# Performance work log

Measured on AMD Instinct MI355X. Metric: run time of the kernel, lower is better.

## Reference

```python
import jax, jax.numpy as jnp
import numpy as np

DIM = 512
NUM_HEADS = 8
HEAD_DIM = DIM // NUM_HEADS
KERNEL = (3, 5, 5)  # (kd, kh, kw), must be odd and <= spatial dims
B, D, H, W = 1, 6, 48, 96


def setup_inputs() -> dict:
    key = jax.random.key(0)
    ks = jax.random.split(key, 5)
    x = jax.random.normal(ks[0], (B, D, H, W, DIM), jnp.float32)
    w_qkv = jax.random.normal(ks[1], (DIM, 3 * DIM), jnp.float32) * 0.02
    b_qkv = jax.random.normal(ks[2], (3 * DIM,), jnp.float32) * 0.02
    w_proj = jax.random.normal(ks[3], (DIM, DIM), jnp.float32) * 0.02
    b_proj = jax.random.normal(ks[4], (DIM,), jnp.float32) * 0.02
    return {"x": x, "w_qkv": w_qkv, "b_qkv": b_qkv, "w_proj": w_proj, "b_proj": b_proj}


def _nbhd_idx(L, k):
    # NATTEN neighborhood: window of exactly k keys, centered, shifted inward at edges.
    p = jnp.arange(L)
    start = jnp.clip(p - k // 2, 0, L - k)
    return start[:, None] + jnp.arange(k)[None, :]  # [L, k]


def _na3d(q, k, v, kernel):
    # q, k, v: [B, D, H, W, heads, hd]; q pre-scaled.
    kd, kh, kw = kernel
    _, Dd, Hh, Ww, _, _ = q.shape
    idx_d = _nbhd_idx(Dd, kd)
    idx_h = _nbhd_idx(Hh, kh)
    idx_w = _nbhd_idx(Ww, kw)
    offs = jnp.stack(
        jnp.meshgrid(jnp.arange(kd), jnp.arange(kh), jnp.arange(kw), indexing="ij"),
        axis=-1,
    ).reshape(-1, 3)  # [K3, 3]

    def shift(t, o):
        # gather the o-th neighbor of every query position along each spatial axis
        t = jnp.take(t, jnp.take(idx_d, o[0], axis=1), axis=1)
        t = jnp.take(t, jnp.take(idx_h, o[1], axis=1), axis=2)
        t = jnp.take(t, jnp.take(idx_w, o[2], axis=1), axis=3)
        return t

    def score_step(_, o):
        k_s = shift(k, o)
        s = jnp.einsum("bdhwnc,bdhwnc->bdhwn", q, k_s)
        return None, s

    _, scores = jax.lax.scan(score_step, None, offs)  # [K3, B, D, H, W, heads]
    attn = jax.nn.softmax(scores, axis=0)

    def out_step(acc, xs):
        o, a = xs
        v_s = shift(v, o)
        return acc + a[..., None] * v_s, None

    out, _ = jax.lax.scan(out_step, jnp.zeros_like(q), (offs, attn))
    return out


def reference(x, w_qkv, b_qkv, w_proj, b_proj):
    Bb, Dd, Hh, Ww, C = x.shape
    qkv = (x @ w_qkv + b_qkv).reshape(Bb, Dd, Hh, Ww, 3, NUM_HEADS, HEAD_DIM)
    q = qkv[..., 0, :, :]
    k = qkv[..., 1, :, :]
    v = qkv[..., 2, :, :]
    scale = HEAD_DIM ** (-0.5)
    # Faithful to source: module scales q by self.scale, then tuned_na3d applies
    # head_dim**-0.5 again inside the fused kernel -> net q * head_dim**-1.
    q = q * (scale * scale)
    out = _na3d(q, k, v, KERNEL).reshape(Bb, Dd, Hh, Ww, C)
    return out @ w_proj + b_proj
```

## Files before the change

### kernel.cpp

```cpp
#include <hip/hip_runtime.h>

#define DIMC   512
#define NHEADS 8
#define HDIM   64
#define DD     6
#define HHH    48
#define WWW    96
#define NPOS   (DD * HHH * WWW)

typedef unsigned short u16;
typedef __attribute__((ext_vector_type(8))) short bf16x8;
typedef __attribute__((ext_vector_type(4))) float f32x4;

static __device__ __forceinline__ float b2f(u16 u) {
    return __builtin_bit_cast(float, (unsigned)u << 16);
}
static __device__ __forceinline__ u16 f2b(float f) {
    unsigned x = __builtin_bit_cast(unsigned, f);
    return (u16)((x + 0x7fffu + ((x >> 16) & 1u)) >> 16);
}

static __device__ __forceinline__ void gload_lds16(const void* g, void* l) {
    __builtin_amdgcn_global_load_lds((const __attribute__((address_space(1))) void*)g,
                                     (__attribute__((address_space(3))) void*)l, 16, 0, 0);
}

__global__ __launch_bounds__(256) void cvt_all(
    const float* __restrict__ x, const float* __restrict__ w_qkv,
    const float* __restrict__ w_proj, u16* __restrict__ xb,
    u16* __restrict__ wqkvT, u16* __restrict__ wprojT)
{
    const int bid = blockIdx.x;
    const int tid = threadIdx.x;
    if (bid < 13824) {
        const int i = bid * 256 + tid;
        float4 v = reinterpret_cast<const float4*>(x)[i];
        ushort4 o = { f2b(v.x), f2b(v.y), f2b(v.z), f2b(v.w) };
        reinterpret_cast<ushort4*>(xb)[i] = o;
    } else if (bid < 13824 + 3072) {
        const int id = (bid - 13824) * 256 + tid;
        const int nn = id >> 9, kk = id & 511;
        wqkvT[id] = f2b(w_qkv[(size_t)kk * 1536 + nn]);
    } else {
        const int id = (bid - 16896) * 256 + tid;
        const int nn = id >> 9, kk = id & 511;
        wprojT[id] = f2b(w_proj[(size_t)kk * 512 + nn]);
    }
}

__global__ __launch_bounds__(512) void gemm_bf16_mfma(
    const u16* __restrict__ A, int lda,
    const u16* __restrict__ B, int ldb,
    const float* __restrict__ bias, int Kp,
    void* __restrict__ Cout, int ldc, int cmode, int nx)
{
    __shared__ u16 As[256 * 64];
    __shared__ u16 Bs[128 * 64];

    const int tid = threadIdx.x;
    const int l   = tid & 63;
    const int w   = tid >> 6;
    const int wr  = w >> 1;
    const int wc  = w & 1;

    const int cpx = gridDim.x >> 3;
    const int idp = (blockIdx.x & 7) * cpx + (blockIdx.x >> 3);
    const int by  = idp / nx;
    const int bx  = idp - by * nx;
    const int m0  = by * 256;
    const int n0  = bx * 128;

    const int lrow = l >> 3;
    const int swz  = ((l & 7) ^ lrow) * 8;
    const int arow = w * 32 + lrow;
    const int brow = w * 16 + lrow;

    const u16* ga = A + (size_t)(m0 + arow) * lda + swz;
    const u16* gb = B + (size_t)(n0 + brow) * ldb + swz;
    const size_t a8 = (size_t)8 * lda;
    const size_t b8 = (size_t)8 * ldb;
    u16* const la0 = As + w * 2048;
    u16* const lb0 = Bs + w * 1024;

    f32x4 acc[4][4];
#pragma unroll
    for (int i = 0; i < 4; i++)
#pragma unroll
        for (int j = 0; j < 4; j++) acc[i][j] = (f32x4)0.0f;

    const int c   = l & 15;
    const int g   = l >> 4;
    const int lk0 = ((0 * 4 + g) ^ (c & 7)) * 8;
    const int lk1 = ((1 * 4 + g) ^ (c & 7)) * 8;

#pragma unroll 1
    for (int k0 = 0; k0 < Kp; k0 += 64) {
#pragma unroll
        for (int q = 0; q < 4; ++q)
            gload_lds16(ga + q * a8, la0 + q * 512);
#pragma unroll
        for (int q = 0; q < 2; ++q)
            gload_lds16(gb + q * b8, lb0 + q * 512);
        ga += 64; gb += 64;
        __syncthreads();

        {
            bf16x8 af[4], bfr[4];
#pragma unroll
            for (int f = 0; f < 4; f++) {
                af[f]  = *reinterpret_cast<const bf16x8*>(&As[(wr * 64 + f * 16 + c) * 64 + lk0]);
                bfr[f] = *reinterpret_cast<const bf16x8*>(&Bs[(wc * 64 + f * 16 + c) * 64 + lk0]);
            }
#pragma unroll
            for (int i = 0; i < 4; i++)
#pragma unroll
                for (int j = 0; j < 4; j++)
                    acc[i][j] = __builtin_amdgcn_mfma_f32_16x16x32_bf16(af[i], bfr[j], acc[i][j], 0, 0, 0);
        }
        {
            bf16x8 af[4], bfr[4];
#pragma unroll
            for (int f = 0; f < 4; f++) {
                af[f]  = *reinterpret_cast<const bf16x8*>(&As[(wr * 64 + f * 16 + c) * 64 + lk1]);
                bfr[f] = *reinterpret_cast<const bf16x8*>(&Bs[(wc * 64 + f * 16 + c) * 64 + lk1]);
            }
#pragma unroll
            for (int i = 0; i < 4; i++)
#pragma unroll
                for (int j = 0; j < 4; j++)
                    acc[i][j] = __builtin_amdgcn_mfma_f32_16x16x32_bf16(af[i], bfr[j], acc[i][j], 0, 0, 0);
        }
        __syncthreads();
    }

#pragma unroll
    for (int i = 0; i < 4; i++) {
        const int mb = m0 + wr * 64 + i * 16 + g * 4;
#pragma unroll
        for (int j = 0; j < 4; j++) {
            const int n = n0 + wc * 64 + j * 16 + c;
            const float bv = bias[n];
            const float scn = (cmode && n < 512) ? 0.022542110f : 1.0f;
#pragma unroll
            for (int r = 0; r < 4; r++) {
                const float v = (acc[i][j][r] + bv) * scn;
                if (cmode) reinterpret_cast<u16*>(Cout)[(size_t)(mb + r) * ldc + n] = f2b(v);
                else       reinterpret_cast<float*>(Cout)[(size_t)(mb + r) * ldc + n] = v;
            }
        }
    }
}

__global__ __launch_bounds__(512, 4) void na3d_mfma(
    const u16* __restrict__ qkv, u16* __restrict__ attnc)
{
    __shared__ int   rowoff[256];
    __shared__ int   dlt[16];
    __shared__ u16   Vt[NHEADS][64][36];
    __shared__ float ssum_lds[NHEADS][2][16];

    const int bid = blockIdx.x;
    const int x   = bid & 7;
    const int u   = bid >> 3;
    const int twl = u / 36;
    const int r2  = u - twl * 36;
    const int d0  = r2 / 12;
    const int thp = r2 - d0 * 12;
    const int h0  = thp * 4;
    const int w0  = (3 * x + twl) * 4;
    const int sdu = min(max(2 * d0 - 1, 0), DD - 4);
    const int shb = min(max(h0 - 2, 0), HHH - 5);
    const int swb = min(max(w0 - 2, 0), WWW - 5);
    const int ddlt0 = min(max(2 * d0 - 1, 0), DD - 3) - sdu;
    const int ddlt1 = min(max(2 * d0, 0), DD - 3) - sdu;

    const int tid = threadIdx.x;
    if (tid < 256) {
        const int dd = tid >> 6, hh = (tid >> 3) & 7, wu = tid & 7;
        const int row = (sdu + dd) * (HHH * WWW)
                      + min(shb + hh, HHH - 1) * WWW + min(swb + wu, WWW - 1);
        rowoff[tid] = row * 1536;
    }
    if (tid < 16) {
        const int ph = h0 + (tid >> 2), pw = w0 + (tid & 3);
        const int dh = min(max(ph - 2, 0), HHH - 5) - shb;
        const int dw = min(max(pw - 2, 0), WWW - 5) - swb;
        dlt[tid] = (dh << 4) | dw;
    }
    __syncthreads();

    const int head = tid >> 6;
    const int l    = tid & 63;
    const int g    = l >> 4;
    const int c    = l & 15;

    const int qbase = (h0 + (c >> 2)) * WWW + (w0 + (c & 3));
    const u16* qrow0 = qkv + (size_t)((2 * d0)     * (HHH * WWW) + qbase) * 1536 + head * HDIM;
    const u16* qrow1 = qkv + (size_t)((2 * d0 + 1) * (HHH * WWW) + qbase) * 1536 + head * HDIM;
    const bf16x8 qlo0 = *reinterpret_cast<const bf16x8*>(qrow0 + 8 * g);
    const bf16x8 qhi0 = *reinterpret_cast<const bf16x8*>(qrow0 + 32 + 8 * g);
    const bf16x8 qlo1 = *reinterpret_cast<const bf16x8*>(qrow1 + 8 * g);
    const bf16x8 qhi1 = *reinterpret_cast<const bf16x8*>(qrow1 + 32 + 8 * g);
    const int dparts = dlt[c];
    const int dh = dparts >> 4, dw = dparts & 15;

    f32x4 oacc0[4], oacc1[4];
#pragma unroll
    for (int j = 0; j < 4; j++) { oacc0[j] = (f32x4)0.0f; oacc1[j] = (f32x4)0.0f; }
    float ssum0 = 0.0f, ssum1 = 0.0f;

#pragma unroll 1
    for (int s = 0; s < 8; ++s) {
        {
            const int npair = l >> 2;
            const int chq   = l & 3;
#pragma unroll
            for (int rr = 0; rr < 2; ++rr) {
                const int ch8 = 8 * chq + 32 * rr;
                const int2 rp = *reinterpret_cast<const int2*>(&rowoff[s * 32 + 2 * npair]);
                const ushort4* pa = reinterpret_cast<const ushort4*>(qkv + rp.x + 1024 + head * HDIM + ch8);
                const ushort4* pb = reinterpret_cast<const ushort4*>(qkv + rp.y + 1024 + head * HDIM + ch8);
                ushort4 va0 = pa[0], va1 = pa[1];
                ushort4 vb0 = pb[0], vb1 = pb[1];
                const u16* va = reinterpret_cast<const u16*>(&va0);
                const u16* vb = reinterpret_cast<const u16*>(&vb0);
#pragma unroll
                for (int e = 0; e < 4; ++e) {
                    unsigned dwo = (unsigned)va[e] | ((unsigned)vb[e] << 16);
                    *reinterpret_cast<unsigned*>(&Vt[head][ch8 + e][2 * npair]) = dwo;
                }
                const u16* va2 = reinterpret_cast<const u16*>(&va1);
                const u16* vb2 = reinterpret_cast<const u16*>(&vb1);
#pragma unroll
                for (int e = 0; e < 4; ++e) {
                    unsigned dwo = (unsigned)va2[e] | ((unsigned)vb2[e] << 16);
                    *reinterpret_cast<unsigned*>(&Vt[head][ch8 + 4 + e][2 * npair]) = dwo;
                }
            }
        }

        f32x4 sf00 = (f32x4)0.0f, sf01 = (f32x4)0.0f;
        f32x4 sf10 = (f32x4)0.0f, sf11 = (f32x4)0.0f;
        {
            const int ro = rowoff[s * 32 + c];
            const u16* kr = qkv + ro + 512 + head * HDIM;
            const bf16x8 klo = *reinterpret_cast<const bf16x8*>(kr + 8 * g);
            const bf16x8 khi = *reinterpret_cast<const bf16x8*>(kr + 32 + 8 * g);
            sf00 = __builtin_amdgcn_mfma_f32_16x16x32_bf16(klo, qlo0, sf00, 0, 0, 0);
            sf00 = __builtin_amdgcn_mfma_f32_16x16x32_bf16(khi, qhi0, sf00, 0, 0, 0);
            sf01 = __builtin_amdgcn_mfma_f32_16x16x32_bf16(klo, qlo1, sf01, 0, 0, 0);
            sf01 = __builtin_amdgcn_mfma_f32_16x16x32_bf16(khi, qhi1, sf01, 0, 0, 0);
        }
        {
            const int ro = rowoff[s * 32 + 16 + c];
            const u16* kr = qkv + ro + 512 + head * HDIM;
            const bf16x8 klo = *reinterpret_cast<const bf16x8*>(kr + 8 * g);
            const bf16x8 khi = *reinterpret_cast<const bf16x8*>(kr + 32 + 8 * g);
            sf10 = __builtin_amdgcn_mfma_f32_16x16x32_bf16(klo, qlo0, sf10, 0, 0, 0);
            sf10 = __builtin_amdgcn_mfma_f32_16x16x32_bf16(khi, qhi0, sf10, 0, 0, 0);
            sf11 = __builtin_amdgcn_mfma_f32_16x16x32_bf16(klo, qlo1, sf11, 0, 0, 0);
            sf11 = __builtin_amdgcn_mfma_f32_16x16x32_bf16(khi, qhi1, sf11, 0, 0, 0);
        }

        const int sbA  = s * 32 + 4 * g;
        const int sbB  = sbA + 16;
        const int ddA  = sbA >> 6, hhA = (sbA >> 3) & 7, wuA = sbA & 7;
        const int ddB  = sbB >> 6, hhB = (sbB >> 3) & 7, wuB = sbB & 7;
        const bool hvA = ((unsigned)(hhA - dh) < 5u);
        const bool hvB = ((unsigned)(hhB - dh) < 5u);

        unsigned pA0, pB0, pC0, pD0, pA1, pB1, pC1, pD1;
#define EXPPACK(sf, dvA_, pX, pY, SSUM, hv_, wu_) do {                          \
    const bool v_ = (dvA_) && (hv_);                                            \
    const float e0 = (v_ && (unsigned)((wu_) + 0 - dw) < 5u) ? exp2f((sf)[0]) : 0.0f; \
    const float e1 = (v_ && (unsigned)((wu_) + 1 - dw) < 5u) ? exp2f((sf)[1]) : 0.0f; \
    const float e2 = (v_ && (unsigned)((wu_) + 2 - dw) < 5u) ? exp2f((sf)[2]) : 0.0f; \
    const float e3 = (v_ && (unsigned)((wu_) + 3 - dw) < 5u) ? exp2f((sf)[3]) : 0.0f; \
    SSUM += e0 + e1 + e2 + e3;                                                  \
    pX = (unsigned)f2b(e0) | ((unsigned)f2b(e1) << 16);                         \
    pY = (unsigned)f2b(e2) | ((unsigned)f2b(e3) << 16);                         \
} while (0)

        EXPPACK(sf00, ((unsigned)(ddA - ddlt0) < 3u), pA0, pB0, ssum0, hvA, wuA);
        EXPPACK(sf10, ((unsigned)(ddB - ddlt0) < 3u), pC0, pD0, ssum0, hvB, wuB);
        EXPPACK(sf01, ((unsigned)(ddA - ddlt1) < 3u), pA1, pB1, ssum1, hvA, wuA);
        EXPPACK(sf11, ((unsigned)(ddB - ddlt1) < 3u), pC1, pD1, ssum1, hvB, wuB);
#undef EXPPACK

        asm volatile("v_permlane32_swap_b32 %0, %1" : "+v"(pA0), "+v"(pC0));
        asm volatile("v_permlane32_swap_b32 %0, %1" : "+v"(pB0), "+v"(pD0));
        asm volatile("v_permlane16_swap_b32 %0, %1" : "+v"(pA0), "+v"(pC0));
        asm volatile("v_permlane16_swap_b32 %0, %1" : "+v"(pB0), "+v"(pD0));
        asm volatile("v_permlane32_swap_b32 %0, %1" : "+v"(pA1), "+v"(pC1));
        asm volatile("v_permlane32_swap_b32 %0, %1" : "+v"(pB1), "+v"(pD1));
        asm volatile("v_permlane16_swap_b32 %0, %1" : "+v"(pA1), "+v"(pC1));
        asm volatile("v_permlane16_swap_b32 %0, %1" : "+v"(pB1), "+v"(pD1));

        {
            const bf16x8 pf0 = __builtin_bit_cast(bf16x8,
                make_int4((int)pA0, (int)pB0, (int)pC0, (int)pD0));
            const bf16x8 pf1 = __builtin_bit_cast(bf16x8,
                make_int4((int)pA1, (int)pB1, (int)pC1, (int)pD1));
#pragma unroll
            for (int j = 0; j < 4; ++j) {
                const uint2 v01 = *reinterpret_cast<const uint2*>(&Vt[head][16 * j + c][8 * g]);
                const uint2 v23 = *reinterpret_cast<const uint2*>(&Vt[head][16 * j + c][8 * g + 4]);
                const bf16x8 vfrag = __builtin_bit_cast(bf16x8,
                    make_int4((int)v01.x, (int)v01.y, (int)v23.x, (int)v23.y));
                oacc0[j] = __builtin_amdgcn_mfma_f32_16x16x32_bf16(pf0, vfrag, oacc0[j], 0, 0, 0);
                oacc1[j] = __builtin_amdgcn_mfma_f32_16x16x32_bf16(pf1, vfrag, oacc1[j], 0, 0, 0);
            }
        }
    }

    ssum0 += __shfl_xor(ssum0, 16);
    ssum0 += __shfl_xor(ssum0, 32);
    ssum1 += __shfl_xor(ssum1, 16);
    ssum1 += __shfl_xor(ssum1, 32);
    if (l < 16) {
        ssum_lds[head][0][c] = ssum0;
        ssum_lds[head][1][c] = ssum1;
    }
    const f32x4 sums40 = *reinterpret_cast<const f32x4*>(&ssum_lds[head][0][4 * g]);
    const f32x4 sums41 = *reinterpret_cast<const f32x4*>(&ssum_lds[head][1][4 * g]);

    const int obase = (h0 + g) * WWW + w0;
    const int orow0 = (2 * d0)     * (HHH * WWW) + obase;
    const int orow1 = (2 * d0 + 1) * (HHH * WWW) + obase;
#pragma unroll
    for (int r = 0; r < 4; ++r) {
        const float inv0 = 1.0f / sums40[r];
        const float inv1 = 1.0f / sums41[r];
        u16* base0 = attnc + (size_t)(orow0 + r) * 512 + head * HDIM;
        u16* base1 = attnc + (size_t)(orow1 + r) * 512 + head * HDIM;
#pragma unroll
        for (int j = 0; j < 4; ++j) {
            base0[16 * j + c] = f2b(oacc0[j][r] * inv0);
            base1[16 * j + c] = f2b(oacc1[j][r] * inv1);
        }
    }
}

extern "C" void kernel_launch(void* const* d_in, const int* in_sizes, int n_in,
                              void* d_out, int out_size, void* d_ws, size_t ws_size,
                              hipStream_t stream)
{
    const float* x      = (const float*)d_in[0];
    const float* w_qkv  = (const float*)d_in[1];
    const float* b_qkv  = (const float*)d_in[2];
    const float* w_proj = (const float*)d_in[3];
    const float* b_proj = (const float*)d_in[4];
    float* out = (float*)d_out;

    u16* qkvb   = (u16*)d_ws;
    u16* attnc  = qkvb  + (size_t)NPOS * 1536;
    u16* xb     = attnc + (size_t)NPOS * 512;
    u16* wqkvT  = xb    + (size_t)NPOS * 512;
    u16* wprojT = wqkvT + (size_t)1536 * 512;

    cvt_all<<<17920, 256, 0, stream>>>(x, w_qkv, w_proj, xb, wqkvT, wprojT);

    gemm_bf16_mfma<<<(NPOS / 256) * (1536 / 128), 512, 0, stream>>>(
        xb, 512, wqkvT, 512, b_qkv, 512, qkvb, 1536, 1, 1536 / 128);

    na3d_mfma<<<NPOS / 32, 512, 0, stream>>>(qkvb, attnc);

    gemm_bf16_mfma<<<(NPOS / 256) * (512 / 128), 512, 0, stream>>>(
        attnc, 512, wprojT, 512, b_proj, 512, out, 512, 0, 512 / 128);
}
```

Baseline: 154.0 us.

## Double-buffer GEMM LDS tiles with K=32 steps to overlap loads and MFMA

Rewrites the bf16 MFMA GEMM main loop to use two LDS buffers of K=32 instead of one K=64 buffer. The next tile's global-to-LDS load is issued before the current tile's MFMAs, so memory latency can overlap compute and there is one barrier per step instead of two. The staging address mapping and XOR swizzle change to fit 32-wide rows. Total LDS stays the same, but each step does half as much MFMA work per barrier. Correctness depends on the barrier at the end of each step ordering both the async load and the reuse of the buffer.

```diff
diff --git a/kernel.cpp b/kernel.cpp
--- a/kernel.cpp
+++ b/kernel.cpp
@@ -54,8 +54,8 @@
     const float* __restrict__ bias, int Kp,
     void* __restrict__ Cout, int ldc, int cmode, int nx)
 {
-    __shared__ u16 As[256 * 64];
-    __shared__ u16 Bs[128 * 64];
+    __shared__ u16 As[2][256 * 32];
+    __shared__ u16 Bs[2][128 * 32];
 
     const int tid = threadIdx.x;
     const int l   = tid & 63;
@@ -70,17 +70,13 @@
     const int m0  = by * 256;
     const int n0  = bx * 128;
 
-    const int lrow = l >> 3;
-    const int swz  = ((l & 7) ^ lrow) * 8;
-    const int arow = w * 32 + lrow;
-    const int brow = w * 16 + lrow;
-
-    const u16* ga = A + (size_t)(m0 + arow) * lda + swz;
-    const u16* gb = B + (size_t)(n0 + brow) * ldb + swz;
-    const size_t a8 = (size_t)8 * lda;
-    const size_t b8 = (size_t)8 * ldb;
-    u16* const la0 = As + w * 2048;
-    u16* const lb0 = Bs + w * 1024;
+    const int srow = tid >> 2;
+    const int schk = ((tid & 3) ^ ((tid >> 3) & 3)) * 8;
+
+    const u16* ga = A + (size_t)(m0 + srow) * lda + schk;
+    const u16* gb = B + (size_t)(n0 + srow) * ldb + schk;
+    const size_t a128 = (size_t)128 * lda;
+    const int sdst = w * 512 + l * 8;
 
     f32x4 acc[4][4];
 #pragma unroll
@@ -88,50 +84,42 @@
 #pragma unroll
         for (int j = 0; j < 4; j++) acc[i][j] = (f32x4)0.0f;
 
-    const int c   = l & 15;
-    const int g   = l >> 4;
-    const int lk0 = ((0 * 4 + g) ^ (c & 7)) * 8;
-    const int lk1 = ((1 * 4 + g) ^ (c & 7)) * 8;
+    const int c  = l & 15;
+    const int g  = l >> 4;
+    const int lk = (g ^ ((c >> 1) & 3)) * 8;
+
+#define STG(buf, kt) do {                                                      \
+    const size_t ko = (size_t)(kt) * 32;                                       \
+    gload_lds16(ga + ko,        &As[buf][sdst]);                               \
+    gload_lds16(ga + a128 + ko, &As[buf][128 * 32 + sdst]);                    \
+    gload_lds16(gb + ko,        &Bs[buf][sdst]);                               \
+} while (0)
+
+    const int nsteps = Kp >> 5;
+
+    STG(0, 0);
+    __syncthreads();
 
 #pragma unroll 1
-    for (int k0 = 0; k0 < Kp; k0 += 64) {
-#pragma unroll
-        for (int q = 0; q < 4; ++q)
-            gload_lds16(ga + q * a8, la0 + q * 512);
-#pragma unroll
-        for (int q = 0; q < 2; ++q)
-            gload_lds16(gb + q * b8, lb0 + q * 512);
-        ga += 64; gb += 64;
+    for (int k = 0; k < nsteps; ++k) {
+        const int cur = k & 1;
+        if (k + 1 < nsteps) STG(cur ^ 1, k + 1);
+
+        bf16x8 af[4], bfr[4];
+#pragma unroll
+        for (int f = 0; f < 4; f++) {
+            af[f]  = *reinterpret_cast<const bf16x8*>(&As[cur][(wr * 64 + f * 16 + c) * 32 + lk]);
+            bfr[f] = *reinterpret_cast<const bf16x8*>(&Bs[cur][(wc * 64 + f * 16 + c) * 32 + lk]);
+        }
+#pragma unroll
+        for (int i = 0; i < 4; i++)
+#pragma unroll
+            for (int j = 0; j < 4; j++)
+                acc[i][j] = __builtin_amdgcn_mfma_f32_16x16x32_bf16(af[i], bfr[j], acc[i][j], 0, 0, 0);
+
         __syncthreads();
-
-        {
-            bf16x8 af[4], bfr[4];
-#pragma unroll
-            for (int f = 0; f < 4; f++) {
-                af[f]  = *reinterpret_cast<const bf16x8*>(&As[(wr * 64 + f * 16 + c) * 64 + lk0]);
-                bfr[f] = *reinterpret_cast<const bf16x8*>(&Bs[(wc * 64 + f * 16 + c) * 64 + lk0]);
-            }
-#pragma unroll
-            for (int i = 0; i < 4; i++)
-#pragma unroll
-                for (int j = 0; j < 4; j++)
-                    acc[i][j] = __builtin_amdgcn_mfma_f32_16x16x32_bf16(af[i], bfr[j], acc[i][j], 0, 0, 0);
-        }
-        {
-            bf16x8 af[4], bfr[4];
-#pragma unroll
-            for (int f = 0; f < 4; f++) {
-                af[f]  = *reinterpret_cast<const bf16x8*>(&As[(wr * 64 + f * 16 + c) * 64 + lk1]);
-                bfr[f] = *reinterpret_cast<const bf16x8*>(&Bs[(wc * 64 + f * 16 + c) * 64 + lk1]);
-            }
-#pragma unroll
-            for (int i = 0; i < 4; i++)
-#pragma unroll
-                for (int j = 0; j < 4; j++)
-                    acc[i][j] = __builtin_amdgcn_mfma_f32_16x16x32_bf16(af[i], bfr[j], acc[i][j], 0, 0, 0);
-        }
-        __syncthreads();
-    }
+    }
+#undef STG
 
 #pragma unroll
     for (int i = 0; i < 4; i++) {
```

Result: slower. 158.6 us (+3.0%).
